# Kernel optimization log

Measured on AMD Instinct MI355X. Metric: run time of the kernel, lower is better.

The kernel has to match this reference:

```python
import jax, jax.numpy as jnp
import numpy as np

HEAD_DIM = 64  # config['head_dim']
# dropout_prob=0.1 is a no-op in eval mode; reference computes deterministic attention.

def setup_inputs() -> dict:
    key = jax.random.key(0)
    kq, kk, kv = jax.random.split(key, 3)
    shape = (2, 12, 2048, HEAD_DIM)  # [batch, heads, seq, head_dim]
    Q = jax.random.normal(kq, shape, dtype=jnp.float32)
    K = jax.random.normal(kk, shape, dtype=jnp.float32)
    V = jax.random.normal(kv, shape, dtype=jnp.float32)
    return {"Q": Q, "K": K, "V": V}

def reference(Q, K, V):
    # dot = Q @ K^T / sqrt(head_dim); attn = softmax(dot); X = attn @ V
    scale = 1.0 / np.float32(np.sqrt(HEAD_DIM))
    dot = jnp.einsum('bhqd,bhkd->bhqk', Q, K) * scale  # [B,H,S,S]
    attn = jax.nn.softmax(dot, axis=-1)
    X = jnp.einsum('bhqk,bhkd->bhqd', attn, V)
    return X
```

## Files before the change

kernel.cpp:

```cpp
#include <hip/hip_runtime.h>
#include <hip/hip_bf16.h>

typedef __attribute__((ext_vector_type(8))) short bf16x8;
typedef __attribute__((ext_vector_type(4))) float f32x4;
typedef __attribute__((ext_vector_type(4))) unsigned short u16x4;
typedef __attribute__((ext_vector_type(2))) unsigned int u32x2;
typedef __attribute__((ext_vector_type(4))) unsigned int u32x4;
typedef __attribute__((ext_vector_type(4))) _Float16 f16x4;
typedef __attribute__((ext_vector_type(8))) _Float16 f16x8;
typedef __attribute__((ext_vector_type(2))) __fp16 h16x2;
typedef __attribute__((ext_vector_type(4))) __fp16 h16x4;

#define SEQ 2048
#define HD 64
#define BH 24

__device__ __forceinline__ unsigned bfpack(float a, float b) {
  union { float f; unsigned u; } ua, ub; ua.f = a; ub.f = b;
  return __builtin_amdgcn_perm(ub.u + 0x8000u, ua.u + 0x8000u, 0x07060302u);
}
__device__ __forceinline__ unsigned short f2bf(float f) {
  union { float f; unsigned u; } v; v.f = f;
  unsigned r = v.u + 0x7fffu + ((v.u >> 16) & 1u);
  return (unsigned short)(r >> 16);
}

__global__ __launch_bounds__(256) void prep_kv(const float* __restrict__ K,
                                               const float* __restrict__ V,
                                               unsigned* __restrict__ Kb,
                                               _Float16* __restrict__ Vt) {
  __shared__ _Float16 t[64 * 68];
  const int bh = blockIdx.y;
  const int k0 = blockIdx.x * 64;
  const int tid = threadIdx.x;

  const float4* ks = (const float4*)(K + ((size_t)bh * SEQ + k0) * HD);
  unsigned* kd = Kb + ((size_t)bh * SEQ + k0) * (HD / 2);
#pragma unroll
  for (int i = 0; i < 4; ++i) {
    int f = tid + i * 256;
    float4 v = ks[f];
    u32x2 o;
    o.x = bfpack(v.x, v.y);
    o.y = bfpack(v.z, v.w);
    *(u32x2*)&kd[f * 2] = o;
  }

  const float4* vs = (const float4*)(V + ((size_t)bh * SEQ + k0) * HD);
#pragma unroll
  for (int i = 0; i < 4; ++i) {
    int f = tid + i * 256;
    int k = f >> 4, cg = f & 15;
    float4 v = vs[k * 16 + cg];
    int dg = cg * 4;
    t[(dg + 0) * 68 + k] = (_Float16)v.x;
    t[(dg + 1) * 68 + k] = (_Float16)v.y;
    t[(dg + 2) * 68 + k] = (_Float16)v.z;
    t[(dg + 3) * 68 + k] = (_Float16)v.w;
  }
  __syncthreads();
  int d = tid >> 2, kg = (tid & 3) * 16;
  _Float16* g = Vt + ((size_t)(bh * 64 + d)) * SEQ + k0 + kg;
#pragma unroll
  for (int r = 0; r < 4; ++r) {
    f16x4 x = *(f16x4*)&t[d * 68 + kg + r * 4];
    *(f16x4*)&g[r * 4] = x;
  }
}

__global__ __launch_bounds__(256, 3) void attn_main(const float* __restrict__ Q,
                                                    const unsigned short* __restrict__ Kb,
                                                    const _Float16* __restrict__ Vt,
                                                    float* __restrict__ O) {
  __shared__ unsigned short kv[3][8192];

  const int tid  = threadIdx.x;
  const int lane = tid & 63;
  const int w    = tid >> 6;
  const int quad = lane >> 4;
  const int n    = lane & 15;

  const int bh = blockIdx.x;
  const int q0 = blockIdx.y * 64;

  const float qscale = 0.125f * 1.44269504088896f;

  bf16x8 qf[4][2];
#pragma unroll
  for (int u = 0; u < 4; ++u) {
    const float* qb = Q + ((size_t)bh * SEQ + q0 + u * 16 + n) * HD;
#pragma unroll
    for (int h = 0; h < 2; ++h) {
      float4 a = *(const float4*)(qb + h * 32 + quad * 8);
      float4 b = *(const float4*)(qb + h * 32 + quad * 8 + 4);
      u32x4 pk;
      pk.x = bfpack(a.x * qscale, a.y * qscale);
      pk.y = bfpack(a.z * qscale, a.w * qscale);
      pk.z = bfpack(b.x * qscale, b.y * qscale);
      pk.w = bfpack(b.z * qscale, b.w * qscale);
      qf[u][h] = __builtin_bit_cast(bf16x8, pk);
    }
  }

  const unsigned short* Kbase = Kb + (size_t)bh * SEQ * HD;
  const unsigned short* Vbase = (const unsigned short*)(Vt + (size_t)bh * HD * SEQ);
  const unsigned short* ksrc[2];
  const unsigned short* vsrc[2];
  int soff[2];
#pragma unroll
  for (int i = 0; i < 2; ++i) {
    int s = i * 256 + tid;
    int r = s >> 3, p = s & 7, G = p ^ (r & 7);
    ksrc[i] = Kbase + r * HD + G * 8;
    vsrc[i] = Vbase + (size_t)r * SEQ + G * 8;
    soff[i] = s * 8;
  }

#define DMA_TO(buf_, it_)                                                                 \
  {                                                                                       \
    unsigned short* db_ = &kv[buf_][0];                                                   \
    _Pragma("unroll")                                                                     \
    for (int i_ = 0; i_ < 2; ++i_) {                                                      \
      __builtin_amdgcn_global_load_lds(                                                   \
          (const __attribute__((address_space(1))) void*)(ksrc[i_] + (size_t)(it_) * 4096), \
          (__attribute__((address_space(3))) void*)(db_ + soff[i_]), 16, 0, 0);           \
      __builtin_amdgcn_global_load_lds(                                                   \
          (const __attribute__((address_space(1))) void*)(vsrc[i_] + (size_t)(it_) * 64), \
          (__attribute__((address_space(3))) void*)(db_ + 4096 + soff[i_]), 16, 0, 0);    \
    }                                                                                     \
    asm volatile("" ::: "memory");                                                        \
  }

  f32x4 o[4][4];
#pragma unroll
  for (int dt = 0; dt < 4; ++dt)
#pragma unroll
    for (int u = 0; u < 4; ++u) o[dt][u] = (f32x4){0.f, 0.f, 0.f, 0.f};
  float lsum[4] = {0.f, 0.f, 0.f, 0.f};

  int ro[2];
#pragma unroll
  for (int h = 0; h < 2; ++h) ro[h] = n * 64 + (((h * 4 + quad) ^ (n & 7)) * 8);
  int vo[4];
#pragma unroll
  for (int dt = 0; dt < 4; ++dt)
    vo[dt] = dt * 1024 + n * 64 + (((w * 2 + (quad >> 1)) ^ (n & 7)) * 8) + (quad & 1) * 4;

#define COMPUTE(buf_)                                                                     \
  {                                                                                       \
    const unsigned short* kb = &kv[buf_][0];                                              \
    const unsigned short* vb = kb + 4096;                                                 \
    f32x4 s[4] = {{0,0,0,0},{0,0,0,0},{0,0,0,0},{0,0,0,0}};                               \
    _Pragma("unroll")                                                                     \
    for (int h = 0; h < 2; ++h) {                                                         \
      bf16x8 a = *(const bf16x8*)&kb[w * 1024 + ro[h]];                                   \
      _Pragma("unroll")                                                                   \
      for (int u = 0; u < 4; ++u)                                                         \
        s[u] = __builtin_amdgcn_mfma_f32_16x16x32_bf16(a, qf[u][h], s[u], 0, 0, 0);       \
    }                                                                                     \
    f16x4 pf[4];                                                                          \
    _Pragma("unroll")                                                                     \
    for (int u = 0; u < 4; ++u) {                                                         \
      float e0 = __builtin_amdgcn_exp2f(s[u][0]);                                         \
      float e1 = __builtin_amdgcn_exp2f(s[u][1]);                                         \
      float e2 = __builtin_amdgcn_exp2f(s[u][2]);                                         \
      float e3 = __builtin_amdgcn_exp2f(s[u][3]);                                         \
      lsum[u] += (e0 + e1) + (e2 + e3);                                                   \
      h16x2 a_ = __builtin_amdgcn_cvt_pkrtz(e0, e1);                                      \
      h16x2 b_ = __builtin_amdgcn_cvt_pkrtz(e2, e3);                                      \
      h16x4 ab_ = __builtin_shufflevector(a_, b_, 0, 1, 2, 3);                            \
      pf[u] = __builtin_bit_cast(f16x4, ab_);                                             \
    }                                                                                     \
    _Pragma("unroll")                                                                     \
    for (int dt = 0; dt < 4; ++dt) {                                                      \
      f16x4 vf = *(const f16x4*)((const _Float16*)vb + vo[dt]);                           \
      _Pragma("unroll")                                                                   \
      for (int u = 0; u < 4; ++u)                                                         \
        o[dt][u] = __builtin_amdgcn_mfma_f32_16x16x16f16(vf, pf[u], o[dt][u], 0, 0, 0);   \
    }                                                                                     \
  }

  DMA_TO(0, 0);
  DMA_TO(1, 1);

  int bc = 0;
  int bd = 2;
  for (int it = 0; it < 31; ++it) {
    asm volatile("s_waitcnt vmcnt(4)\n\ts_barrier" ::: "memory");
    if (it < 30) DMA_TO(bd, it + 2);
    COMPUTE(bc);
    bc = (bc == 2) ? 0 : bc + 1;
    bd = (bd == 2) ? 0 : bd + 1;
  }
  asm volatile("s_waitcnt vmcnt(0)\n\ts_barrier" ::: "memory");
  COMPUTE(bc);

#undef DMA_TO
#undef COMPUTE

#pragma unroll
  for (int u = 0; u < 4; ++u) {
    lsum[u] += __shfl_xor(lsum[u], 16);
    lsum[u] += __shfl_xor(lsum[u], 32);
  }

  float* red = (float*)&kv[0][0];
  float* lred = red + 2 * 4096;

  __syncthreads();
  if (w & 1) {
    int s = w >> 1;
#pragma unroll
    for (int dt = 0; dt < 4; ++dt)
#pragma unroll
      for (int u = 0; u < 4; ++u)
        *(f32x4*)&red[s * 4096 + (dt * 4 + u) * 256 + lane * 4] = o[dt][u];
#pragma unroll
    for (int u = 0; u < 4; ++u) lred[s * 256 + u * 64 + lane] = lsum[u];
  }
  __syncthreads();
  if (!(w & 1)) {
    int s = w >> 1;
#pragma unroll
    for (int dt = 0; dt < 4; ++dt)
#pragma unroll
      for (int u = 0; u < 4; ++u)
        o[dt][u] += *(f32x4*)&red[s * 4096 + (dt * 4 + u) * 256 + lane * 4];
#pragma unroll
    for (int u = 0; u < 4; ++u) lsum[u] += lred[s * 256 + u * 64 + lane];
  }
  __syncthreads();
  if (w == 2) {
#pragma unroll
    for (int dt = 0; dt < 4; ++dt)
#pragma unroll
      for (int u = 0; u < 4; ++u)
        *(f32x4*)&red[4096 + (dt * 4 + u) * 256 + lane * 4] = o[dt][u];
#pragma unroll
    for (int u = 0; u < 4; ++u) lred[256 + u * 64 + lane] = lsum[u];
  }
  __syncthreads();
  if (w == 0) {
#pragma unroll
    for (int dt = 0; dt < 4; ++dt)
#pragma unroll
      for (int u = 0; u < 4; ++u)
        o[dt][u] += *(f32x4*)&red[4096 + (dt * 4 + u) * 256 + lane * 4];
#pragma unroll
    for (int u = 0; u < 4; ++u) {
      float inv = 1.0f / (lsum[u] + lred[256 + u * 64 + lane]);
      float* og = O + ((size_t)bh * SEQ + q0 + u * 16 + n) * HD + quad * 4;
#pragma unroll
      for (int dt = 0; dt < 4; ++dt) {
        f32x4 r = o[dt][u];
        r.x *= inv; r.y *= inv; r.z *= inv; r.w *= inv;
        *(f32x4*)(og + dt * 16) = r;
      }
    }
  }
}

#define F_QT 128
#define F_KT 64
#define F_LD 72

__global__ __launch_bounds__(512) void attn_fwd(const float* __restrict__ Q,
                                                const float* __restrict__ K,
                                                const float* __restrict__ V,
                                                float* __restrict__ O) {
  __shared__ unsigned short sm[(F_QT + F_KT + HD + 8 * 16) * F_LD];
  unsigned short* Qs = sm;
  unsigned short* Ks = Qs + F_QT * F_LD;
  unsigned short* Vt = Ks + F_KT * F_LD;
  unsigned short* Ps = Vt + HD * F_LD;

  const int tid = threadIdx.x, lane = tid & 63, wv = tid >> 6;
  const int quad = lane >> 4, n = lane & 15;
  const int bh = blockIdx.y, q0 = blockIdx.x * F_QT;
  const float* Qg = Q + ((size_t)bh * SEQ + q0) * HD;
  const float* Kg = K + (size_t)bh * SEQ * HD;
  const float* Vg = V + (size_t)bh * SEQ * HD;
  float* Og = O + ((size_t)bh * SEQ + q0) * HD;
  const float qscale = 0.125f * 1.44269504088896f;

#pragma unroll
  for (int i = 0; i < 4; ++i) {
    int f = tid + i * 512;
    int row = f >> 4, cg = f & 15;
    float4 qv = ((const float4*)Qg)[row * 16 + cg];
    u16x4 h;
    h.x = f2bf(qv.x * qscale); h.y = f2bf(qv.y * qscale);
    h.z = f2bf(qv.z * qscale); h.w = f2bf(qv.w * qscale);
    *(u16x4*)&Qs[row * F_LD + cg * 4] = h;
  }
  __syncthreads();
  bf16x8 qf0 = *(const bf16x8*)&Qs[(wv * 16 + n) * F_LD + quad * 8];
  bf16x8 qf1 = *(const bf16x8*)&Qs[(wv * 16 + n) * F_LD + 32 + quad * 8];
  f32x4 o[4] = {{0,0,0,0},{0,0,0,0},{0,0,0,0},{0,0,0,0}};
  float mrow[4] = {-1e30f,-1e30f,-1e30f,-1e30f};
  float lrow[4] = {0.f,0.f,0.f,0.f};
  unsigned short* Pw = Ps + wv * 16 * F_LD;

  for (int it = 0; it < SEQ / F_KT; ++it) {
    __syncthreads();
    const float* Ktg = Kg + (size_t)it * F_KT * HD;
    const float* Vtg = Vg + (size_t)it * F_KT * HD;
#pragma unroll
    for (int i = 0; i < 2; ++i) {
      int f = tid + i * 512;
      int row = f >> 4, cg = f & 15;
      float4 kvv = ((const float4*)Ktg)[row * 16 + cg];
      u16x4 hk;
      hk.x = f2bf(kvv.x); hk.y = f2bf(kvv.y); hk.z = f2bf(kvv.z); hk.w = f2bf(kvv.w);
      *(u16x4*)&Ks[row * F_LD + cg * 4] = hk;
      float4 vv = ((const float4*)Vtg)[row * 16 + cg];
      Vt[(cg * 4 + 0) * F_LD + row] = f2bf(vv.x);
      Vt[(cg * 4 + 1) * F_LD + row] = f2bf(vv.y);
      Vt[(cg * 4 + 2) * F_LD + row] = f2bf(vv.z);
      Vt[(cg * 4 + 3) * F_LD + row] = f2bf(vv.w);
    }
    __syncthreads();
    f32x4 s[4];
#pragma unroll
    for (int t = 0; t < 4; ++t) {
      bf16x8 b0 = *(const bf16x8*)&Ks[(t * 16 + n) * F_LD + quad * 8];
      bf16x8 b1 = *(const bf16x8*)&Ks[(t * 16 + n) * F_LD + 32 + quad * 8];
      f32x4 c = {0,0,0,0};
      c = __builtin_amdgcn_mfma_f32_16x16x32_bf16(qf0, b0, c, 0, 0, 0);
      c = __builtin_amdgcn_mfma_f32_16x16x32_bf16(qf1, b1, c, 0, 0, 0);
      s[t] = c;
    }
    float mnew[4], alpha[4], rsum[4];
#pragma unroll
    for (int r = 0; r < 4; ++r) {
      float ml = fmaxf(fmaxf(s[0][r], s[1][r]), fmaxf(s[2][r], s[3][r]));
      ml = fmaxf(ml, __shfl_xor(ml, 1));
      ml = fmaxf(ml, __shfl_xor(ml, 2));
      ml = fmaxf(ml, __shfl_xor(ml, 4));
      ml = fmaxf(ml, __shfl_xor(ml, 8));
      mnew[r] = fmaxf(mrow[r], ml);
      alpha[r] = __builtin_amdgcn_exp2f(mrow[r] - mnew[r]);
      mrow[r] = mnew[r];
      rsum[r] = 0.f;
    }
#pragma unroll
    for (int t = 0; t < 4; ++t)
#pragma unroll
      for (int r = 0; r < 4; ++r) {
        float p = __builtin_amdgcn_exp2f(s[t][r] - mnew[r]);
        rsum[r] += p;
        Pw[(quad * 4 + r) * F_LD + t * 16 + n] = f2bf(p);
      }
#pragma unroll
    for (int r = 0; r < 4; ++r) {
      float rs = rsum[r];
      rs += __shfl_xor(rs, 1); rs += __shfl_xor(rs, 2);
      rs += __shfl_xor(rs, 4); rs += __shfl_xor(rs, 8);
      lrow[r] = lrow[r] * alpha[r] + rs;
      o[0][r] *= alpha[r]; o[1][r] *= alpha[r];
      o[2][r] *= alpha[r]; o[3][r] *= alpha[r];
    }
    asm volatile("s_waitcnt lgkmcnt(0)" ::: "memory");
    bf16x8 p0 = *(const bf16x8*)&Pw[n * F_LD + quad * 8];
    bf16x8 p1 = *(const bf16x8*)&Pw[n * F_LD + 32 + quad * 8];
#pragma unroll
    for (int t = 0; t < 4; ++t) {
      bf16x8 v0 = *(const bf16x8*)&Vt[(t * 16 + n) * F_LD + quad * 8];
      bf16x8 v1 = *(const bf16x8*)&Vt[(t * 16 + n) * F_LD + 32 + quad * 8];
      o[t] = __builtin_amdgcn_mfma_f32_16x16x32_bf16(p0, v0, o[t], 0, 0, 0);
      o[t] = __builtin_amdgcn_mfma_f32_16x16x32_bf16(p1, v1, o[t], 0, 0, 0);
    }
  }
  float inv[4];
#pragma unroll
  for (int r = 0; r < 4; ++r) inv[r] = 1.0f / lrow[r];
#pragma unroll
  for (int t = 0; t < 4; ++t)
#pragma unroll
    for (int r = 0; r < 4; ++r)
      Og[(wv * 16 + quad * 4 + r) * HD + t * 16 + n] = o[t][r] * inv[r];
}

extern "C" void kernel_launch(void* const* d_in, const int* in_sizes, int n_in,
                              void* d_out, int out_size, void* d_ws, size_t ws_size,
                              hipStream_t stream) {
  const float* Q = (const float*)d_in[0];
  const float* K = (const float*)d_in[1];
  const float* V = (const float*)d_in[2];
  float* O = (float*)d_out;

  const size_t mat = (size_t)BH * SEQ * HD;
  const size_t need = 2 * mat * sizeof(unsigned short);

  if (ws_size >= need) {
    unsigned short* Kb = (unsigned short*)d_ws;
    _Float16* Vt = (_Float16*)(Kb + mat);
    prep_kv<<<dim3(SEQ / 64, BH), 256, 0, stream>>>(K, V, (unsigned*)Kb, Vt);
    attn_main<<<dim3(BH, SEQ / 64), 256, 0, stream>>>(Q, Kb, Vt, O);
  } else {
    attn_fwd<<<dim3(SEQ / F_QT, BH), 512, 0, stream>>>(Q, K, V, O);
  }
}
```

Baseline: 119.4 us.

## Use 32x32x16 MFMA for PV and remap blocks XCD-aware across heads

The P·V product now uses 32x32x16 f16 MFMA instead of 16x16x16, rearranging the P fragments with ds_swizzle lane exchanges and loading V as 8-wide fragments. This cuts the MFMA instruction count and V LDS reads per tile. The launch grid is flattened, and block IDs are remapped so each group of 8 consecutive blocks (one per XCD) covers a set of heads, aiming for better L2 locality of K/V per XCD. The cost is extra swizzle and select instructions, plus a reworked reduction and epilogue layout.

```diff
diff --git a/kernel.cpp b/kernel.cpp
--- a/kernel.cpp
+++ b/kernel.cpp
@@ -3,6 +3,7 @@
 
 typedef __attribute__((ext_vector_type(8))) short bf16x8;
 typedef __attribute__((ext_vector_type(4))) float f32x4;
+typedef __attribute__((ext_vector_type(16))) float f32x16;
 typedef __attribute__((ext_vector_type(4))) unsigned short u16x4;
 typedef __attribute__((ext_vector_type(2))) unsigned int u32x2;
 typedef __attribute__((ext_vector_type(4))) unsigned int u32x4;
@@ -30,8 +31,10 @@
                                                unsigned* __restrict__ Kb,
                                                _Float16* __restrict__ Vt) {
   __shared__ _Float16 t[64 * 68];
-  const int bh = blockIdx.y;
-  const int k0 = blockIdx.x * 64;
+  const int bid = blockIdx.x;
+  const int sb = bid >> 3;
+  const int bh = (bid & 7) * 3 + (sb >> 5);
+  const int k0 = (sb & 31) * 64;
   const int tid = threadIdx.x;
 
   const float4* ks = (const float4*)(K + ((size_t)bh * SEQ + k0) * HD);
@@ -79,9 +82,12 @@
   const int w    = tid >> 6;
   const int quad = lane >> 4;
   const int n    = lane & 15;
-
-  const int bh = blockIdx.x;
-  const int q0 = blockIdx.y * 64;
+  const bool hi16 = (lane & 16) != 0;
+
+  const int bid = blockIdx.x;
+  const int sb = bid >> 3;
+  const int bh = (bid & 7) * 3 + (sb >> 5);
+  const int q0 = (sb & 31) * 64;
 
   const float qscale = 0.125f * 1.44269504088896f;
 
@@ -131,25 +137,25 @@
     asm volatile("" ::: "memory");                                                        \
   }
 
-  f32x4 o[4][4];
-#pragma unroll
-  for (int dt = 0; dt < 4; ++dt)
-#pragma unroll
-    for (int u = 0; u < 4; ++u) o[dt][u] = (f32x4){0.f, 0.f, 0.f, 0.f};
+  f32x16 oacc[2][2];
+#pragma unroll
+  for (int d_ = 0; d_ < 2; ++d_)
+#pragma unroll
+    for (int g_ = 0; g_ < 2; ++g_) oacc[d_][g_] = (f32x16)(0.f);
   float lsum[4] = {0.f, 0.f, 0.f, 0.f};
 
   int ro[2];
 #pragma unroll
   for (int h = 0; h < 2; ++h) ro[h] = n * 64 + (((h * 4 + quad) ^ (n & 7)) * 8);
-  int vo[4];
-#pragma unroll
-  for (int dt = 0; dt < 4; ++dt)
-    vo[dt] = dt * 1024 + n * 64 + (((w * 2 + (quad >> 1)) ^ (n & 7)) * 8) + (quad & 1) * 4;
+  int vaoff[2];
+#pragma unroll
+  for (int d_ = 0; d_ < 2; ++d_)
+    vaoff[d_] = (d_ * 32 + (lane & 31)) * 64 + (((w * 2 + (lane >> 5)) ^ (lane & 7)) * 8);
 
 #define COMPUTE(buf_)                                                                     \
   {                                                                                       \
     const unsigned short* kb = &kv[buf_][0];                                              \
-    const unsigned short* vb = kb + 4096;                                                 \
+    const _Float16* vb = (const _Float16*)(kb + 4096);                                    \
     f32x4 s[4] = {{0,0,0,0},{0,0,0,0},{0,0,0,0},{0,0,0,0}};                               \
     _Pragma("unroll")                                                                     \
     for (int h = 0; h < 2; ++h) {                                                         \
@@ -158,7 +164,9 @@
       for (int u = 0; u < 4; ++u)                                                         \
         s[u] = __builtin_amdgcn_mfma_f32_16x16x32_bf16(a, qf[u][h], s[u], 0, 0, 0);       \
     }                                                                                     \
-    f16x4 pf[4];                                                                          \
+    f16x8 va0 = *(const f16x8*)&vb[vaoff[0]];                                             \
+    f16x8 va1 = *(const f16x8*)&vb[vaoff[1]];                                             \
+    unsigned pc0[4], pc1[4];                                                              \
     _Pragma("unroll")                                                                     \
     for (int u = 0; u < 4; ++u) {                                                         \
       float e0 = __builtin_amdgcn_exp2f(s[u][0]);                                         \
@@ -168,15 +176,25 @@
       lsum[u] += (e0 + e1) + (e2 + e3);                                                   \
       h16x2 a_ = __builtin_amdgcn_cvt_pkrtz(e0, e1);                                      \
       h16x2 b_ = __builtin_amdgcn_cvt_pkrtz(e2, e3);                                      \
-      h16x4 ab_ = __builtin_shufflevector(a_, b_, 0, 1, 2, 3);                            \
-      pf[u] = __builtin_bit_cast(f16x4, ab_);                                             \
+      pc0[u] = __builtin_bit_cast(unsigned, a_);                                          \
+      pc1[u] = __builtin_bit_cast(unsigned, b_);                                          \
     }                                                                                     \
     _Pragma("unroll")                                                                     \
-    for (int dt = 0; dt < 4; ++dt) {                                                      \
-      f16x4 vf = *(const f16x4*)((const _Float16*)vb + vo[dt]);                           \
-      _Pragma("unroll")                                                                   \
-      for (int u = 0; u < 4; ++u)                                                         \
-        o[dt][u] = __builtin_amdgcn_mfma_f32_16x16x16f16(vf, pf[u], o[dt][u], 0, 0, 0);   \
+    for (int qg = 0; qg < 2; ++qg) {                                                      \
+      unsigned A0 = pc0[qg * 2], A1 = pc0[qg * 2 + 1];                                    \
+      unsigned B0 = pc1[qg * 2], B1 = pc1[qg * 2 + 1];                                    \
+      unsigned S0 = (unsigned)__builtin_amdgcn_ds_swizzle((int)A0, 0x401F);               \
+      unsigned S1 = (unsigned)__builtin_amdgcn_ds_swizzle((int)A1, 0x401F);               \
+      unsigned T0 = (unsigned)__builtin_amdgcn_ds_swizzle((int)B0, 0x401F);               \
+      unsigned T1 = (unsigned)__builtin_amdgcn_ds_swizzle((int)B1, 0x401F);               \
+      u32x4 pw;                                                                           \
+      pw.x = hi16 ? S1 : A0;                                                              \
+      pw.y = hi16 ? T1 : B0;                                                              \
+      pw.z = hi16 ? A1 : S0;                                                              \
+      pw.w = hi16 ? B1 : T0;                                                              \
+      f16x8 pb = __builtin_bit_cast(f16x8, pw);                                           \
+      oacc[0][qg] = __builtin_amdgcn_mfma_f32_32x32x16_f16(va0, pb, oacc[0][qg], 0, 0, 0);\
+      oacc[1][qg] = __builtin_amdgcn_mfma_f32_32x32x16_f16(va1, pb, oacc[1][qg], 0, 0, 0);\
     }                                                                                     \
   }
 
@@ -209,52 +227,83 @@
 
   __syncthreads();
   if (w & 1) {
-    int s = w >> 1;
-#pragma unroll
-    for (int dt = 0; dt < 4; ++dt)
-#pragma unroll
-      for (int u = 0; u < 4; ++u)
-        *(f32x4*)&red[s * 4096 + (dt * 4 + u) * 256 + lane * 4] = o[dt][u];
-#pragma unroll
-    for (int u = 0; u < 4; ++u) lred[s * 256 + u * 64 + lane] = lsum[u];
+    int sl = w >> 1;
+#pragma unroll
+    for (int f = 0; f < 4; ++f) {
+      const int d_ = f >> 1, g_ = f & 1;
+#pragma unroll
+      for (int rq = 0; rq < 4; ++rq) {
+        f32x4 ch = {oacc[d_][g_][rq * 4 + 0], oacc[d_][g_][rq * 4 + 1],
+                    oacc[d_][g_][rq * 4 + 2], oacc[d_][g_][rq * 4 + 3]};
+        *(f32x4*)&red[sl * 4096 + (f * 4 + rq) * 256 + lane * 4] = ch;
+      }
+    }
+#pragma unroll
+    for (int u = 0; u < 4; ++u) lred[sl * 256 + u * 64 + lane] = lsum[u];
   }
   __syncthreads();
   if (!(w & 1)) {
-    int s = w >> 1;
-#pragma unroll
-    for (int dt = 0; dt < 4; ++dt)
-#pragma unroll
-      for (int u = 0; u < 4; ++u)
-        o[dt][u] += *(f32x4*)&red[s * 4096 + (dt * 4 + u) * 256 + lane * 4];
-#pragma unroll
-    for (int u = 0; u < 4; ++u) lsum[u] += lred[s * 256 + u * 64 + lane];
+    int sl = w >> 1;
+#pragma unroll
+    for (int f = 0; f < 4; ++f) {
+      const int d_ = f >> 1, g_ = f & 1;
+#pragma unroll
+      for (int rq = 0; rq < 4; ++rq) {
+        f32x4 ch = *(f32x4*)&red[sl * 4096 + (f * 4 + rq) * 256 + lane * 4];
+        oacc[d_][g_][rq * 4 + 0] += ch.x;
+        oacc[d_][g_][rq * 4 + 1] += ch.y;
+        oacc[d_][g_][rq * 4 + 2] += ch.z;
+        oacc[d_][g_][rq * 4 + 3] += ch.w;
+      }
+    }
+#pragma unroll
+    for (int u = 0; u < 4; ++u) lsum[u] += lred[sl * 256 + u * 64 + lane];
   }
   __syncthreads();
   if (w == 2) {
 #pragma unroll
-    for (int dt = 0; dt < 4; ++dt)
-#pragma unroll
-      for (int u = 0; u < 4; ++u)
-        *(f32x4*)&red[4096 + (dt * 4 + u) * 256 + lane * 4] = o[dt][u];
+    for (int f = 0; f < 4; ++f) {
+      const int d_ = f >> 1, g_ = f & 1;
+#pragma unroll
+      for (int rq = 0; rq < 4; ++rq) {
+        f32x4 ch = {oacc[d_][g_][rq * 4 + 0], oacc[d_][g_][rq * 4 + 1],
+                    oacc[d_][g_][rq * 4 + 2], oacc[d_][g_][rq * 4 + 3]};
+        *(f32x4*)&red[4096 + (f * 4 + rq) * 256 + lane * 4] = ch;
+      }
+    }
 #pragma unroll
     for (int u = 0; u < 4; ++u) lred[256 + u * 64 + lane] = lsum[u];
   }
   __syncthreads();
   if (w == 0) {
 #pragma unroll
-    for (int dt = 0; dt < 4; ++dt)
-#pragma unroll
-      for (int u = 0; u < 4; ++u)
-        o[dt][u] += *(f32x4*)&red[4096 + (dt * 4 + u) * 256 + lane * 4];
-#pragma unroll
-    for (int u = 0; u < 4; ++u) {
-      float inv = 1.0f / (lsum[u] + lred[256 + u * 64 + lane]);
-      float* og = O + ((size_t)bh * SEQ + q0 + u * 16 + n) * HD + quad * 4;
-#pragma unroll
-      for (int dt = 0; dt < 4; ++dt) {
-        f32x4 r = o[dt][u];
-        r.x *= inv; r.y *= inv; r.z *= inv; r.w *= inv;
-        *(f32x4*)(og + dt * 16) = r;
+    for (int f = 0; f < 4; ++f) {
+      const int d_ = f >> 1, g_ = f & 1;
+#pragma unroll
+      for (int rq = 0; rq < 4; ++rq) {
+        f32x4 ch = *(f32x4*)&red[4096 + (f * 4 + rq) * 256 + lane * 4];
+        oacc[d_][g_][rq * 4 + 0] += ch.x;
+        oacc[d_][g_][rq * 4 + 1] += ch.y;
+        oacc[d_][g_][rq * 4 + 2] += ch.z;
+        oacc[d_][g_][rq * 4 + 3] += ch.w;
+      }
+    }
+    float L[4];
+#pragma unroll
+    for (int u = 0; u < 4; ++u) L[u] = lsum[u] + lred[256 + u * 64 + lane];
+    const int l31 = lane & 31, hb = lane >> 5;
+#pragma unroll
+    for (int g_ = 0; g_ < 2; ++g_) {
+      const float iv = (lane & 16) ? 1.0f / L[g_ * 2 + 1] : 1.0f / L[g_ * 2];
+#pragma unroll
+      for (int d_ = 0; d_ < 2; ++d_) {
+        float* og = O + ((size_t)bh * SEQ + q0 + g_ * 32 + l31) * HD + d_ * 32 + 4 * hb;
+#pragma unroll
+        for (int rq = 0; rq < 4; ++rq) {
+          f32x4 r = {oacc[d_][g_][rq * 4 + 0] * iv, oacc[d_][g_][rq * 4 + 1] * iv,
+                     oacc[d_][g_][rq * 4 + 2] * iv, oacc[d_][g_][rq * 4 + 3] * iv};
+          *(f32x4*)(og + 8 * rq) = r;
+        }
       }
     }
   }
@@ -395,8 +444,8 @@
   if (ws_size >= need) {
     unsigned short* Kb = (unsigned short*)d_ws;
     _Float16* Vt = (_Float16*)(Kb + mat);
-    prep_kv<<<dim3(SEQ / 64, BH), 256, 0, stream>>>(K, V, (unsigned*)Kb, Vt);
-    attn_main<<<dim3(BH, SEQ / 64), 256, 0, stream>>>(Q, Kb, Vt, O);
+    prep_kv<<<dim3(SEQ / 64 * BH), 256, 0, stream>>>(K, V, (unsigned*)Kb, Vt);
+    attn_main<<<dim3(BH * SEQ / 64), 256, 0, stream>>>(Q, Kb, Vt, O);
   } else {
     attn_fwd<<<dim3(SEQ / F_QT, BH), 512, 0, stream>>>(Q, K, V, O);
   }
```

Measured after the change: 121.5 us. Within noise of the previous version (+1.7%).

## Switch attn_main to double-buffered K/V tiles to raise occupancy to five blocks

Applied to the files above, without the earlier changes.

Shrinks the shared-memory K/V ring from three buffers to two and raises the launch-bounds occupancy hint from 3 to 5 blocks per CU. The loop now prefetches only one tile ahead and waits for all outstanding loads before each compute step. The final cross-wave reduction is reorganised so the softmax row sums fit in the smaller shared buffer. More resident blocks are meant to hide latency better, but the shallower prefetch exposes more load latency per iteration and the tighter register budget may cause spills.

```diff
diff --git a/kernel.cpp b/kernel.cpp
--- a/kernel.cpp
+++ b/kernel.cpp
@@ -7,7 +7,6 @@
 typedef __attribute__((ext_vector_type(2))) unsigned int u32x2;
 typedef __attribute__((ext_vector_type(4))) unsigned int u32x4;
 typedef __attribute__((ext_vector_type(4))) _Float16 f16x4;
-typedef __attribute__((ext_vector_type(8))) _Float16 f16x8;
 typedef __attribute__((ext_vector_type(2))) __fp16 h16x2;
 typedef __attribute__((ext_vector_type(4))) __fp16 h16x4;
 
@@ -68,11 +67,11 @@
   }
 }
 
-__global__ __launch_bounds__(256, 3) void attn_main(const float* __restrict__ Q,
+__global__ __launch_bounds__(256, 5) void attn_main(const float* __restrict__ Q,
                                                     const unsigned short* __restrict__ Kb,
                                                     const _Float16* __restrict__ Vt,
                                                     float* __restrict__ O) {
-  __shared__ unsigned short kv[3][8192];
+  __shared__ unsigned short kv[2][8192];
 
   const int tid  = threadIdx.x;
   const int lane = tid & 63;
@@ -181,19 +180,12 @@
   }
 
   DMA_TO(0, 0);
-  DMA_TO(1, 1);
-
-  int bc = 0;
-  int bd = 2;
-  for (int it = 0; it < 31; ++it) {
-    asm volatile("s_waitcnt vmcnt(4)\n\ts_barrier" ::: "memory");
-    if (it < 30) DMA_TO(bd, it + 2);
-    COMPUTE(bc);
-    bc = (bc == 2) ? 0 : bc + 1;
-    bd = (bd == 2) ? 0 : bd + 1;
-  }
-  asm volatile("s_waitcnt vmcnt(0)\n\ts_barrier" ::: "memory");
-  COMPUTE(bc);
+
+  for (int it = 0; it < 32; ++it) {
+    asm volatile("s_waitcnt vmcnt(0)\n\ts_barrier" ::: "memory");
+    if (it < 31) DMA_TO((it + 1) & 1, it + 1);
+    COMPUTE(it & 1);
+  }
 
 #undef DMA_TO
 #undef COMPUTE
@@ -205,39 +197,54 @@
   }
 
   float* red = (float*)&kv[0][0];
-  float* lred = red + 2 * 4096;
+
+  __syncthreads();
+  if (w == 1) {
+#pragma unroll
+    for (int u = 0; u < 4; ++u) red[u * 64 + lane] = lsum[u];
+  }
+  if (w == 3) {
+#pragma unroll
+    for (int u = 0; u < 4; ++u) red[256 + u * 64 + lane] = lsum[u];
+  }
+  __syncthreads();
+  if (w == 0) {
+#pragma unroll
+    for (int u = 0; u < 4; ++u) lsum[u] += red[u * 64 + lane];
+  }
+  if (w == 2) {
+#pragma unroll
+    for (int u = 0; u < 4; ++u) lsum[u] += red[256 + u * 64 + lane];
+  }
 
   __syncthreads();
   if (w & 1) {
-    int s = w >> 1;
+    int sl = w >> 1;
 #pragma unroll
     for (int dt = 0; dt < 4; ++dt)
 #pragma unroll
       for (int u = 0; u < 4; ++u)
-        *(f32x4*)&red[s * 4096 + (dt * 4 + u) * 256 + lane * 4] = o[dt][u];
-#pragma unroll
-    for (int u = 0; u < 4; ++u) lred[s * 256 + u * 64 + lane] = lsum[u];
+        *(f32x4*)&red[sl * 4096 + (dt * 4 + u) * 256 + lane * 4] = o[dt][u];
   }
   __syncthreads();
   if (!(w & 1)) {
-    int s = w >> 1;
+    int sl = w >> 1;
 #pragma unroll
     for (int dt = 0; dt < 4; ++dt)
 #pragma unroll
       for (int u = 0; u < 4; ++u)
-        o[dt][u] += *(f32x4*)&red[s * 4096 + (dt * 4 + u) * 256 + lane * 4];
-#pragma unroll
-    for (int u = 0; u < 4; ++u) lsum[u] += lred[s * 256 + u * 64 + lane];
-  }
+        o[dt][u] += *(f32x4*)&red[sl * 4096 + (dt * 4 + u) * 256 + lane * 4];
+  }
+
   __syncthreads();
   if (w == 2) {
 #pragma unroll
     for (int dt = 0; dt < 4; ++dt)
 #pragma unroll
       for (int u = 0; u < 4; ++u)
-        *(f32x4*)&red[4096 + (dt * 4 + u) * 256 + lane * 4] = o[dt][u];
-#pragma unroll
-    for (int u = 0; u < 4; ++u) lred[256 + u * 64 + lane] = lsum[u];
+        *(f32x4*)&red[(dt * 4 + u) * 256 + lane * 4] = o[dt][u];
+#pragma unroll
+    for (int u = 0; u < 4; ++u) red[4096 + u * 64 + lane] = lsum[u];
   }
   __syncthreads();
   if (w == 0) {
@@ -245,10 +252,10 @@
     for (int dt = 0; dt < 4; ++dt)
 #pragma unroll
       for (int u = 0; u < 4; ++u)
-        o[dt][u] += *(f32x4*)&red[4096 + (dt * 4 + u) * 256 + lane * 4];
+        o[dt][u] += *(f32x4*)&red[(dt * 4 + u) * 256 + lane * 4];
 #pragma unroll
     for (int u = 0; u < 4; ++u) {
-      float inv = 1.0f / (lsum[u] + lred[256 + u * 64 + lane]);
+      float inv = 1.0f / (lsum[u] + red[4096 + u * 64 + lane]);
       float* og = O + ((size_t)bh * SEQ + q0 + u * 16 + n) * HD + quad * 4;
 #pragma unroll
       for (int dt = 0; dt < 4; ++dt) {
```

After: 265.1 us. +122.0%, slower.

## Software-pipeline QK^T of next tile with softmax and PV of current

Applied to the files above, without the earlier changes.

Splits the per-tile compute into a QK^T part and an exp/PV part, then issues the next tile's QK^T MFMAs before the current tile's exponentials and PV MFMAs. The intent is to overlap transcendental ALU work with matrix-core work and hide MFMA latency. The loop is unrolled by two with rotating buffer indices. An extra barrier is added before each DMA into the freed buffer, and two score register sets raise register pressure.

```diff
diff --git a/kernel.cpp b/kernel.cpp
--- a/kernel.cpp
+++ b/kernel.cpp
@@ -7,7 +7,6 @@
 typedef __attribute__((ext_vector_type(2))) unsigned int u32x2;
 typedef __attribute__((ext_vector_type(4))) unsigned int u32x4;
 typedef __attribute__((ext_vector_type(4))) _Float16 f16x4;
-typedef __attribute__((ext_vector_type(8))) _Float16 f16x8;
 typedef __attribute__((ext_vector_type(2))) __fp16 h16x2;
 typedef __attribute__((ext_vector_type(4))) __fp16 h16x4;
 
@@ -146,25 +145,30 @@
   for (int dt = 0; dt < 4; ++dt)
     vo[dt] = dt * 1024 + n * 64 + (((w * 2 + (quad >> 1)) ^ (n & 7)) * 8) + (quad & 1) * 4;
 
-#define COMPUTE(buf_)                                                                     \
+#define QK_PART(kbp_, sd_)                                                                \
   {                                                                                       \
-    const unsigned short* kb = &kv[buf_][0];                                              \
-    const unsigned short* vb = kb + 4096;                                                 \
-    f32x4 s[4] = {{0,0,0,0},{0,0,0,0},{0,0,0,0},{0,0,0,0}};                               \
+    const unsigned short* kb = (kbp_);                                                    \
+    sd_[0] = (f32x4){0,0,0,0}; sd_[1] = (f32x4){0,0,0,0};                                 \
+    sd_[2] = (f32x4){0,0,0,0}; sd_[3] = (f32x4){0,0,0,0};                                 \
     _Pragma("unroll")                                                                     \
     for (int h = 0; h < 2; ++h) {                                                         \
       bf16x8 a = *(const bf16x8*)&kb[w * 1024 + ro[h]];                                   \
       _Pragma("unroll")                                                                   \
       for (int u = 0; u < 4; ++u)                                                         \
-        s[u] = __builtin_amdgcn_mfma_f32_16x16x32_bf16(a, qf[u][h], s[u], 0, 0, 0);       \
+        sd_[u] = __builtin_amdgcn_mfma_f32_16x16x32_bf16(a, qf[u][h], sd_[u], 0, 0, 0);   \
     }                                                                                     \
+  }
+
+#define SMPV_PART(ss_, kbp_)                                                              \
+  {                                                                                       \
+    const unsigned short* vb = (kbp_) + 4096;                                             \
     f16x4 pf[4];                                                                          \
     _Pragma("unroll")                                                                     \
     for (int u = 0; u < 4; ++u) {                                                         \
-      float e0 = __builtin_amdgcn_exp2f(s[u][0]);                                         \
-      float e1 = __builtin_amdgcn_exp2f(s[u][1]);                                         \
-      float e2 = __builtin_amdgcn_exp2f(s[u][2]);                                         \
-      float e3 = __builtin_amdgcn_exp2f(s[u][3]);                                         \
+      float e0 = __builtin_amdgcn_exp2f(ss_[u][0]);                                       \
+      float e1 = __builtin_amdgcn_exp2f(ss_[u][1]);                                       \
+      float e2 = __builtin_amdgcn_exp2f(ss_[u][2]);                                       \
+      float e3 = __builtin_amdgcn_exp2f(ss_[u][3]);                                       \
       lsum[u] += (e0 + e1) + (e2 + e3);                                                   \
       h16x2 a_ = __builtin_amdgcn_cvt_pkrtz(e0, e1);                                      \
       h16x2 b_ = __builtin_amdgcn_cvt_pkrtz(e2, e3);                                      \
@@ -180,23 +184,38 @@
     }                                                                                     \
   }
 
+  f32x4 sA[4], sB[4];
+
   DMA_TO(0, 0);
   DMA_TO(1, 1);
-
-  int bc = 0;
-  int bd = 2;
-  for (int it = 0; it < 31; ++it) {
+  asm volatile("s_waitcnt vmcnt(4)\n\ts_barrier" ::: "memory");
+  DMA_TO(2, 2);
+  QK_PART(&kv[0][0], sA);
+
+  int bb0 = 0, bb1 = 1, bb2 = 2;
+  for (int t = 0; t < 15; ++t) {
+    const int it1 = 2 * t + 1;
     asm volatile("s_waitcnt vmcnt(4)\n\ts_barrier" ::: "memory");
-    if (it < 30) DMA_TO(bd, it + 2);
-    COMPUTE(bc);
-    bc = (bc == 2) ? 0 : bc + 1;
-    bd = (bd == 2) ? 0 : bd + 1;
-  }
+    QK_PART(&kv[bb1][0], sB);
+    SMPV_PART(sA, &kv[bb0][0]);
+    asm volatile("s_barrier" ::: "memory");
+    DMA_TO(bb0, it1 + 2);
+    asm volatile("s_waitcnt vmcnt(4)\n\ts_barrier" ::: "memory");
+    QK_PART(&kv[bb2][0], sA);
+    SMPV_PART(sB, &kv[bb1][0]);
+    asm volatile("s_barrier" ::: "memory");
+    if (t < 14) DMA_TO(bb1, it1 + 3);
+    int tmp = bb2; bb2 = bb1; bb1 = bb0; bb0 = tmp;
+  }
+
   asm volatile("s_waitcnt vmcnt(0)\n\ts_barrier" ::: "memory");
-  COMPUTE(bc);
+  QK_PART(&kv[1][0], sB);
+  SMPV_PART(sA, &kv[0][0]);
+  SMPV_PART(sB, &kv[1][0]);
 
 #undef DMA_TO
-#undef COMPUTE
+#undef QK_PART
+#undef SMPV_PART
 
 #pragma unroll
   for (int u = 0; u < 4; ++u) {
```

Measured after the change: 211.2 us. +76.8%, slower.
